# Kernel tuning notes

Hardware: AMD Instinct MI355X
Metric: run time of the kernel (lower is better)

The kernel has to match this reference:

```python
import jax, jax.numpy as jnp
import numpy as np

T, B, D = 2048, 2, 768
H = 8
HD = D // H
FFN = 3072
EPS = 1e-5


def layer_norm(x, g, b):
    mu = jnp.mean(x, axis=-1, keepdims=True)
    var = jnp.mean(jnp.square(x - mu), axis=-1, keepdims=True)
    return (x - mu) * jax.lax.rsqrt(var + EPS) * g + b


def setup_inputs() -> dict:
    key = jax.random.key(0)
    ks = jax.random.split(key, 12)
    s_d = 1.0 / np.sqrt(D)
    s_f = 1.0 / np.sqrt(FFN)
    return {
        "x": jax.random.normal(ks[0], (T, B, D), dtype=jnp.float32),
        "wq": jax.random.uniform(ks[1], (D, D), jnp.float32, -s_d, s_d),
        "bq": jnp.zeros((D,), jnp.float32),
        "wk": jax.random.uniform(ks[2], (D, D), jnp.float32, -s_d, s_d),
        "bk": jnp.zeros((D,), jnp.float32),
        "wv": jax.random.uniform(ks[3], (D, D), jnp.float32, -s_d, s_d),
        "bv": jnp.zeros((D,), jnp.float32),
        "wo": jax.random.uniform(ks[4], (D, D), jnp.float32, -s_d, s_d),
        "bo": jnp.zeros((D,), jnp.float32),
        "ln1_g": jnp.ones((D,), jnp.float32),
        "ln1_b": jnp.zeros((D,), jnp.float32),
        "w1": jax.random.uniform(ks[5], (FFN, D), jnp.float32, -s_d, s_d),
        "b1": jnp.zeros((FFN,), jnp.float32),
        "w2": jax.random.uniform(ks[6], (D, FFN), jnp.float32, -s_f, s_f),
        "b2": jnp.zeros((D,), jnp.float32),
        "ln2_g": jnp.ones((D,), jnp.float32),
        "ln2_b": jnp.zeros((D,), jnp.float32),
    }


def reference(x, wq, bq, wk, bk, wv, bv, wo, bo, ln1_g, ln1_b, w1, b1, w2, b2, ln2_g, ln2_b):
    # x: [T, B, D] (fairseq layout). Post-LN (layer_norm_first=False), relu, eval mode.
    residual = x
    q = (x @ wq.T + bq).reshape(T, B, H, HD)
    k = (x @ wk.T + bk).reshape(T, B, H, HD)
    v = (x @ wv.T + bv).reshape(T, B, H, HD)
    scale = 1.0 / np.sqrt(HD)
    scores = jnp.einsum('tbhd,sbhd->bhts', q, k) * scale  # [B,H,T,T]
    probs = jax.nn.softmax(scores, axis=-1)
    attn = jnp.einsum('bhts,sbhd->tbhd', probs, v).reshape(T, B, D)
    attn = attn @ wo.T + bo
    x = layer_norm(residual + attn, ln1_g, ln1_b)
    residual = x
    h = jax.nn.relu(x @ w1.T + b1)
    x = residual + (h @ w2.T + b2)
    x = layer_norm(x, ln2_g, ln2_b)
    return x
```

## Files before the change

### kernel.cpp

```cpp
#include <hip/hip_runtime.h>
#include <hip/hip_bf16.h>
#include <math.h>

constexpr int T_LEN = 2048;
constexpr int B_SZ  = 2;
constexpr int D_DIM = 768;
constexpr int H_NUM = 8;
constexpr int HD    = 96;
constexpr int FFN   = 3072;
constexpr float EPS = 1e-5f;
constexpr int TB    = T_LEN * B_SZ;
constexpr int QKV_LD = 3 * D_DIM;
constexpr int NSPLIT = 4;
constexpr int CHUNK  = T_LEN / NSPLIT;
constexpr float SC_LOG2E = 0.14724444458547f;

typedef __attribute__((ext_vector_type(8)))  short short8;
typedef __attribute__((ext_vector_type(4)))  short short4v;
typedef __attribute__((ext_vector_type(2)))  short short2v;
typedef __attribute__((ext_vector_type(4)))  float f32x4;
typedef __attribute__((ext_vector_type(16))) float f32x16;

__device__ __forceinline__ short f2bf(float f) {
    union { float f; unsigned u; } v; v.f = f;
    return (short)((v.u + 0x7FFFu + ((v.u >> 16) & 1u)) >> 16);
}
__device__ __forceinline__ float bf2f(short s) {
    union { unsigned u; float f; } v;
    v.u = ((unsigned)(unsigned short)s) << 16;
    return v.f;
}
__device__ __forceinline__ unsigned pkbf(float a, float b) {
    union { __hip_bfloat162 h; unsigned u; } v;
    v.h = __float22bfloat162_rn(make_float2(a, b));
    return v.u;
}

__device__ __forceinline__ void async_ld16(const short* g, short* l) {
    __builtin_amdgcn_global_load_lds(
        (const __attribute__((address_space(1))) unsigned int*)g,
        (__attribute__((address_space(3))) unsigned int*)l, 16, 0, 0);
}

struct CvtArgs {
    const float* src[7];
    short*       dst[7];
    float        scl[7];
    int          end4[7];
};

__global__ __launch_bounds__(256)
void cvt_all(CvtArgs a, int total4) {
    const int i = blockIdx.x * 256 + threadIdx.x;
    if (i >= total4) return;
    int s = 0;
    while (i >= a.end4[s]) ++s;
    const int base = s ? a.end4[s - 1] : 0;
    const int j = i - base;
    const float sc = a.scl[s];
    const float4 v = ((const float4*)a.src[s])[j];
    short4v o;
    o[0] = f2bf(v.x * sc); o[1] = f2bf(v.y * sc);
    o[2] = f2bf(v.z * sc); o[3] = f2bf(v.w * sc);
    *(short4v*)(a.dst[s] + (size_t)j * 4) = o;
}

__global__ __launch_bounds__(256)
void concat_bias(const float* __restrict__ bq, const float* __restrict__ bk,
                 const float* __restrict__ bv, float* __restrict__ dst) {
    const int i = blockIdx.x * 256 + threadIdx.x;
    if (i >= QKV_LD) return;
    dst[i] = (i < 768) ? bq[i] * SC_LOG2E : (i < 1536 ? bk[i - 768] : bv[i - 1536]);
}

template <int BM, int BN, typename OutT, bool RELU>
__global__ __launch_bounds__(256)
void gemm_mfma(const short* __restrict__ A, const short* __restrict__ W,
               const float* __restrict__ bias, OutT* __restrict__ C,
               int M, int N, int K) {
    constexpr int MI = BM / 32;
    constexpr int NI = BN / 32;
    __shared__ __align__(16) short As[BM * 32];
    __shared__ __align__(16) short Bs[BN * 32];

    const int tid  = threadIdx.x;
    const int w    = tid >> 6;
    const int lane = tid & 63;
    const int l16  = lane & 15;
    const int q4   = lane >> 4;
    const int row0 = blockIdx.y * BM;
    const int col0 = blockIdx.x * BN;
    const int wm   = (w >> 1) * (BM / 2);
    const int wn   = (w & 1) * (BN / 2);

    const short* gA0 = A + (size_t)(row0 + (tid >> 2)) * K + (tid & 3) * 8;
    const short* gA1 = gA0 + (size_t)64 * K;
    const short* gB0 = W + (size_t)(col0 + (tid >> 2)) * K + (tid & 3) * 8;
    const short* gB1 = gB0 + (size_t)64 * K;
    short* ldsA0 = As + w * 512;
    short* ldsA1 = As + 2048 + w * 512;
    short* ldsB0 = Bs + w * 512;
    short* ldsB1 = Bs + 2048 + w * 512;

    f32x4 acc[MI][NI];
#pragma unroll
    for (int mi = 0; mi < MI; ++mi)
#pragma unroll
        for (int ni = 0; ni < NI; ++ni)
#pragma unroll
            for (int r = 0; r < 4; ++r) acc[mi][ni][r] = 0.f;

    for (int k0 = 0; k0 < K; k0 += 32) {
        async_ld16(gA0, ldsA0);
        if constexpr (BM == 128) async_ld16(gA1, ldsA1);
        async_ld16(gB0, ldsB0);
        if constexpr (BN == 128) async_ld16(gB1, ldsB1);
        gA0 += 32; gB0 += 32;
        if constexpr (BM == 128) gA1 += 32;
        if constexpr (BN == 128) gB1 += 32;
        __syncthreads();

        short8 af[MI], bfr[NI];
#pragma unroll
        for (int mi = 0; mi < MI; ++mi)
            af[mi] = *(const short8*)&As[(wm + mi * 16 + l16) * 32 + q4 * 8];
#pragma unroll
        for (int ni = 0; ni < NI; ++ni)
            bfr[ni] = *(const short8*)&Bs[(wn + ni * 16 + l16) * 32 + q4 * 8];
#pragma unroll
        for (int mi = 0; mi < MI; ++mi)
#pragma unroll
            for (int ni = 0; ni < NI; ++ni)
                acc[mi][ni] = __builtin_amdgcn_mfma_f32_16x16x32_bf16(
                    af[mi], bfr[ni], acc[mi][ni], 0, 0, 0);
        __syncthreads();
    }

    float bcol[NI];
#pragma unroll
    for (int ni = 0; ni < NI; ++ni) bcol[ni] = bias[col0 + wn + ni * 16 + l16];
#pragma unroll
    for (int mi = 0; mi < MI; ++mi) {
#pragma unroll
        for (int r = 0; r < 4; ++r) {
            const int row = row0 + wm + mi * 16 + q4 * 4 + r;
#pragma unroll
            for (int ni = 0; ni < NI; ++ni) {
                float v = acc[mi][ni][r] + bcol[ni];
                if (RELU) v = fmaxf(v, 0.f);
                const int col = col0 + wn + ni * 16 + l16;
                if constexpr (sizeof(OutT) == 2)
                    C[(size_t)row * N + col] = (OutT)f2bf(v);
                else
                    C[(size_t)row * N + col] = v;
            }
        }
    }
}

__global__ __launch_bounds__(256)
void attn_mfma(const short* __restrict__ qkv, short* __restrict__ Opart,
               float* __restrict__ lpart) {
    __shared__ short Ks[2][32][56];
    __shared__ short Vt[128][44];
    __shared__ short Pw[4][32][36];

    const int tid  = threadIdx.x;
    const int w    = tid >> 6;
    const int lane = tid & 63;
    const int l31  = lane & 31;
    const int h5   = lane >> 5;
    const int t0   = blockIdx.x * 128;
    const int bh   = blockIdx.y;
    const int split = blockIdx.z;
    const int b    = bh >> 3;
    const int h    = bh & 7;

    for (int i = tid; i < 32 * 44; i += 256) {
        const int rr = i / 44, cc = i % 44;
        Vt[96 + rr][cc] = (rr == 0 && cc < 32) ? (short)0x3F80 : (short)0;
    }

    short8 qf[6];
    {
        const int qrow = t0 + w * 32 + l31;
        const short* qb = qkv + ((size_t)qrow * B_SZ + b) * QKV_LD + h * HD;
#pragma unroll
        for (int ks = 0; ks < 6; ++ks)
            qf[ks] = *(const short8*)&qb[ks * 16 + h5 * 8];
    }

    const int k_row = tid >> 2;
    const int k_q   = tid & 3;
    const short* gK = qkv + ((size_t)(split * CHUNK + k_row) * B_SZ + b) * QKV_LD
                      + D_DIM + h * HD + k_q * 24;
    const int ll = tid - 128;
    const int dg = (ll & 7) * 12;
    const int kg = (ll >> 3) * 2;
    const short* gV = qkv + ((size_t)(split * CHUNK + kg) * B_SZ + b) * QKV_LD
                      + 2 * D_DIM + h * HD + dg;
    const size_t step  = (size_t)32 * B_SZ * QKV_LD;
    const size_t vrow  = (size_t)B_SZ * QKV_LD;

    f32x16 oacc[4];
#pragma unroll
    for (int nt = 0; nt < 4; ++nt)
#pragma unroll
        for (int r = 0; r < 16; ++r) oacc[nt][r] = 0.f;

    short8  kpf[3];
    short4v vpf[2][3];
    if (w < 2) {
#pragma unroll
        for (int j = 0; j < 3; ++j) kpf[j] = *(const short8*)(gK + j * 8);
    } else {
#pragma unroll
        for (int r = 0; r < 2; ++r)
#pragma unroll
            for (int c = 0; c < 3; ++c)
                vpf[r][c] = *(const short4v*)(gV + r * vrow + c * 4);
    }

    for (int it = 0; it < CHUNK / 32; ++it) {
        __syncthreads();
        if (w < 2) {
#pragma unroll
            for (int j = 0; j < 3; ++j)
                *(short8*)&Ks[k_q >> 1][k_row][(k_q & 1) * 24 + j * 8] = kpf[j];
        } else {
#pragma unroll
            for (int d = 0; d < 12; ++d) {
                short2v t;
                t[0] = vpf[0][d >> 2][d & 3];
                t[1] = vpf[1][d >> 2][d & 3];
                *(short2v*)&Vt[dg + d][kg] = t;
            }
        }
        __syncthreads();

        if (it + 1 < CHUNK / 32) {
            const size_t off = (size_t)(it + 1) * step;
            if (w < 2) {
#pragma unroll
                for (int j = 0; j < 3; ++j)
                    kpf[j] = *(const short8*)(gK + off + j * 8);
            } else {
#pragma unroll
                for (int r = 0; r < 2; ++r)
#pragma unroll
                    for (int c = 0; c < 3; ++c)
                        vpf[r][c] = *(const short4v*)(gV + off + r * vrow + c * 4);
            }
        }

        f32x16 sa;
#pragma unroll
        for (int r = 0; r < 16; ++r) sa[r] = 0.f;
#pragma unroll
        for (int ks = 0; ks < 6; ++ks) {
            const int half = ks / 3;
            const int base = ks * 16 - half * 48;
            const short8 kf = *(const short8*)&Ks[half][l31][base + h5 * 8];
            sa = __builtin_amdgcn_mfma_f32_32x32x16_bf16(qf[ks], kf, sa, 0, 0, 0);
        }

        float pvx[16];
#pragma unroll
        for (int r = 0; r < 16; ++r) pvx[r] = __builtin_amdgcn_exp2f(sa[r]);
#pragma unroll
        for (int rp = 0; rp < 8; ++rp) {
            const unsigned u = pkbf(pvx[2 * rp], pvx[2 * rp + 1]);
            const int row = ((2 * rp) & 3) + 8 * ((2 * rp) >> 2) + 4 * h5;
            Pw[w][row][l31]     = (short)(u & 0xFFFFu);
            Pw[w][row + 1][l31] = (short)(u >> 16);
        }

#pragma unroll
        for (int ks2 = 0; ks2 < 2; ++ks2) {
            const short* pp = &Pw[w][l31][ks2 * 16 + h5 * 8];
            const short4v plo = *(const short4v*)pp;
            const short4v phi = *(const short4v*)(pp + 4);
            const short8 pfr = __builtin_shufflevector(plo, phi, 0, 1, 2, 3, 4, 5, 6, 7);
#pragma unroll
            for (int nt = 0; nt < 4; ++nt) {
                const short* vp = &Vt[nt * 32 + l31][ks2 * 16 + h5 * 8];
                const short4v vlo = *(const short4v*)vp;
                const short4v vhi = *(const short4v*)(vp + 4);
                const short8 vf = __builtin_shufflevector(vlo, vhi, 0, 1, 2, 3, 4, 5, 6, 7);
                oacc[nt] = __builtin_amdgcn_mfma_f32_32x32x16_bf16(pfr, vf, oacc[nt], 0, 0, 0);
            }
        }
    }

#pragma unroll
    for (int r = 0; r < 16; ++r) {
        const int row  = (r & 3) + 8 * (r >> 2) + 4 * h5;
        const int t    = t0 + w * 32 + row;
        const int grow = t * B_SZ + b;
        short* op = Opart + ((size_t)split * TB + grow) * D_DIM + h * HD;
#pragma unroll
        for (int nt = 0; nt < 3; ++nt)
            op[nt * 32 + l31] = f2bf(oacc[nt][r]);
        if (l31 == 0)
            lpart[((size_t)split * TB + grow) * H_NUM + h] = oacc[3][r];
    }
}

__global__ __launch_bounds__(256)
void attn_combine(const short* __restrict__ Opart, const float* __restrict__ lpart,
                  short* __restrict__ ctx) {
    const int row = blockIdx.x;
    const int tid = threadIdx.x;
    if (tid >= 192) return;
    const int d = tid * 4;
    const int h = d / 96;
    float o0 = 0.f, o1 = 0.f, o2 = 0.f, o3 = 0.f, l = 0.f;
#pragma unroll
    for (int c = 0; c < NSPLIT; ++c) {
        const short4v v = *(const short4v*)&Opart[((size_t)c * TB + row) * D_DIM + d];
        o0 += bf2f(v[0]); o1 += bf2f(v[1]); o2 += bf2f(v[2]); o3 += bf2f(v[3]);
        l += lpart[((size_t)c * TB + row) * H_NUM + h];
    }
    const float iv = 1.f / l;
    short4v r;
    r[0] = f2bf(o0 * iv); r[1] = f2bf(o1 * iv);
    r[2] = f2bf(o2 * iv); r[3] = f2bf(o3 * iv);
    *(short4v*)&ctx[(size_t)row * D_DIM + d] = r;
}

template <typename XT, typename OT>
__global__ __launch_bounds__(256)
void ln_residual(const XT* __restrict__ xres, const short* __restrict__ y,
                 const float* __restrict__ g, const float* __restrict__ bb,
                 OT* __restrict__ out) {
    const int row = blockIdx.x;
    const int tid = threadIdx.x;
    const XT*    xr = xres + (size_t)row * D_DIM;
    const short* yr = y + (size_t)row * D_DIM;

    float vals[3];
    float s = 0.f, s2 = 0.f;
#pragma unroll
    for (int i = 0; i < 3; ++i) {
        const int d = tid + i * 256;
        float xv;
        if constexpr (sizeof(XT) == 2) xv = bf2f((short)xr[d]);
        else                           xv = (float)xr[d];
        const float t = xv + bf2f(yr[d]);
        vals[i] = t;
        s += t;
        s2 = fmaf(t, t, s2);
    }
#pragma unroll
    for (int off = 32; off > 0; off >>= 1) {
        s  += __shfl_down(s, off);
        s2 += __shfl_down(s2, off);
    }
    __shared__ float red_s[4], red_s2[4];
    const int wid = tid >> 6, lane = tid & 63;
    if (lane == 0) { red_s[wid] = s; red_s2[wid] = s2; }
    __syncthreads();
    __shared__ float sh_mean, sh_rstd;
    if (tid == 0) {
        const float ts  = red_s[0] + red_s[1] + red_s[2] + red_s[3];
        const float ts2 = red_s2[0] + red_s2[1] + red_s2[2] + red_s2[3];
        const float mean = ts * (1.f / D_DIM);
        const float var  = ts2 * (1.f / D_DIM) - mean * mean;
        sh_mean = mean;
        sh_rstd = rsqrtf(var + EPS);
    }
    __syncthreads();
    const float mean = sh_mean, rstd = sh_rstd;
#pragma unroll
    for (int i = 0; i < 3; ++i) {
        const int d = tid + i * 256;
        const float o = (vals[i] - mean) * rstd * g[d] + bb[d];
        if constexpr (sizeof(OT) == 2)
            out[(size_t)row * D_DIM + d] = (OT)f2bf(o);
        else
            out[(size_t)row * D_DIM + d] = o;
    }
}

extern "C" void kernel_launch(void* const* d_in, const int* in_sizes, int n_in,
                              void* d_out, int out_size, void* d_ws, size_t ws_size,
                              hipStream_t stream) {
    const float* x     = (const float*)d_in[0];
    const float* wq    = (const float*)d_in[1];
    const float* bq    = (const float*)d_in[2];
    const float* wk    = (const float*)d_in[3];
    const float* bk    = (const float*)d_in[4];
    const float* wv    = (const float*)d_in[5];
    const float* bv    = (const float*)d_in[6];
    const float* wo    = (const float*)d_in[7];
    const float* bo    = (const float*)d_in[8];
    const float* ln1g  = (const float*)d_in[9];
    const float* ln1b  = (const float*)d_in[10];
    const float* w1    = (const float*)d_in[11];
    const float* b1    = (const float*)d_in[12];
    const float* w2    = (const float*)d_in[13];
    const float* b2    = (const float*)d_in[14];
    const float* ln2g  = (const float*)d_in[15];
    const float* ln2b  = (const float*)d_in[16];
    float* out = (float*)d_out;

    char* ws = (char*)d_ws;
    short* qkvb  = (short*)(ws + 0);
    short* ctxb  = (short*)(ws + 18874368);
    short* hb    = (short*)(ws + 0);
    short* xb    = (short*)(ws + 25165824);
    short* Opart = (short*)(ws + 25165824);
    float* lpart = (float*)(ws + 50331648);
    short* tmpb  = (short*)(ws + 25165824);
    short* x1b   = (short*)(ws + 31457280);
    short* wqkv  = (short*)(ws + 50855936);
    short* wob   = (short*)(ws + 54394880);
    short* w1b   = (short*)(ws + 55574528);
    short* w2b   = (short*)(ws + 60293120);
    float* bqkv  = (float*)(ws + 65011712);

    CvtArgs ca;
    ca.src[0] = x;  ca.dst[0] = xb;   ca.scl[0] = 1.f;
    ca.src[1] = wq; ca.dst[1] = wqkv; ca.scl[1] = SC_LOG2E;
    ca.src[2] = wk; ca.dst[2] = wqkv + 768 * 768;     ca.scl[2] = 1.f;
    ca.src[3] = wv; ca.dst[3] = wqkv + 2 * 768 * 768; ca.scl[3] = 1.f;
    ca.src[4] = wo; ca.dst[4] = wob;  ca.scl[4] = 1.f;
    ca.src[5] = w1; ca.dst[5] = w1b;  ca.scl[5] = 1.f;
    ca.src[6] = w2; ca.dst[6] = w2b;  ca.scl[6] = 1.f;
    const int n4[7] = {TB * D_DIM / 4, 768 * 768 / 4, 768 * 768 / 4, 768 * 768 / 4,
                       768 * 768 / 4, FFN * 768 / 4, 768 * FFN / 4};
    int acc4 = 0;
    for (int i = 0; i < 7; ++i) { acc4 += n4[i]; ca.end4[i] = acc4; }
    cvt_all<<<(acc4 + 255) / 256, 256, 0, stream>>>(ca, acc4);
    concat_bias<<<(QKV_LD + 255) / 256, 256, 0, stream>>>(bq, bk, bv, bqkv);

    gemm_mfma<128, 128, short, false><<<dim3(QKV_LD / 128, TB / 128), 256, 0, stream>>>(
        xb, wqkv, bqkv, qkvb, TB, QKV_LD, D_DIM);

    attn_mfma<<<dim3(T_LEN / 128, B_SZ * H_NUM, NSPLIT), dim3(256), 0, stream>>>(
        qkvb, Opart, lpart);
    attn_combine<<<dim3(TB), 256, 0, stream>>>(Opart, lpart, ctxb);

    gemm_mfma<64, 64, short, false><<<dim3(D_DIM / 64, TB / 64), 256, 0, stream>>>(
        ctxb, wob, bo, tmpb, TB, D_DIM, D_DIM);
    ln_residual<float, short><<<dim3(TB), 256, 0, stream>>>(x, tmpb, ln1g, ln1b, x1b);

    gemm_mfma<128, 128, short, true><<<dim3(FFN / 128, TB / 128), 256, 0, stream>>>(
        x1b, w1b, b1, hb, TB, FFN, D_DIM);
    gemm_mfma<64, 64, short, false><<<dim3(D_DIM / 64, TB / 64), 256, 0, stream>>>(
        hb, w2b, b2, tmpb, TB, D_DIM, FFN);
    ln_residual<short, float><<<dim3(TB), 256, 0, stream>>>(x1b, tmpb, ln2g, ln2b, out);
}
```

Before: 309.7 us.

## Double-buffer GEMM LDS tiles with async prefetch and deeper K for small tiles

Rewrites the GEMM main loop so LDS holds two buffers. The next K tile is issued asynchronously while the current one is computed, with a partial vmcnt wait and raw s_barrier instead of two __syncthreads per step. The 64x64 GEMMs now use BK=64, so every stage moves 4 async loads per thread and there are fewer loop iterations. This hides global load latency behind MFMA work, at the cost of twice the LDS footprint and possible LDS bank conflicts from the wider row stride.

```diff
diff --git a/kernel.cpp b/kernel.cpp
--- a/kernel.cpp
+++ b/kernel.cpp
@@ -73,15 +73,18 @@
     dst[i] = (i < 768) ? bq[i] * SC_LOG2E : (i < 1536 ? bk[i - 768] : bv[i - 1536]);
 }
 
-template <int BM, int BN, typename OutT, bool RELU>
+template <int BM, int BN, int BK, typename OutT, bool RELU>
 __global__ __launch_bounds__(256)
 void gemm_mfma(const short* __restrict__ A, const short* __restrict__ W,
                const float* __restrict__ bias, OutT* __restrict__ C,
                int M, int N, int K) {
     constexpr int MI = BM / 32;
     constexpr int NI = BN / 32;
-    __shared__ __align__(16) short As[BM * 32];
-    __shared__ __align__(16) short Bs[BN * 32];
+    constexpr int KI = BK / 32;
+    static_assert(BM * BK == 4096 && BN * BK == 4096, "4 glds/thread/stage");
+    constexpr int ROWSTEP = 2048 / BK;
+    __shared__ __align__(16) short As[2][4096];
+    __shared__ __align__(16) short Bs[2][4096];
 
     const int tid  = threadIdx.x;
     const int w    = tid >> 6;
@@ -93,14 +96,12 @@
     const int wm   = (w >> 1) * (BM / 2);
     const int wn   = (w & 1) * (BN / 2);
 
-    const short* gA0 = A + (size_t)(row0 + (tid >> 2)) * K + (tid & 3) * 8;
-    const short* gA1 = gA0 + (size_t)64 * K;
-    const short* gB0 = W + (size_t)(col0 + (tid >> 2)) * K + (tid & 3) * 8;
-    const short* gB1 = gB0 + (size_t)64 * K;
-    short* ldsA0 = As + w * 512;
-    short* ldsA1 = As + 2048 + w * 512;
-    short* ldsB0 = Bs + w * 512;
-    short* ldsB1 = Bs + 2048 + w * 512;
+    const int mA = tid / (BK / 8);
+    const int kA = (tid % (BK / 8)) * 8;
+    const short* gA0 = A + (size_t)(row0 + mA) * K + kA;
+    const short* gA1 = gA0 + (size_t)ROWSTEP * K;
+    const short* gB0 = W + (size_t)(col0 + mA) * K + kA;
+    const short* gB1 = gB0 + (size_t)ROWSTEP * K;
 
     f32x4 acc[MI][NI];
 #pragma unroll
@@ -110,30 +111,47 @@
 #pragma unroll
             for (int r = 0; r < 4; ++r) acc[mi][ni][r] = 0.f;
 
-    for (int k0 = 0; k0 < K; k0 += 32) {
-        async_ld16(gA0, ldsA0);
-        if constexpr (BM == 128) async_ld16(gA1, ldsA1);
-        async_ld16(gB0, ldsB0);
-        if constexpr (BN == 128) async_ld16(gB1, ldsB1);
-        gA0 += 32; gB0 += 32;
-        if constexpr (BM == 128) gA1 += 32;
-        if constexpr (BN == 128) gB1 += 32;
-        __syncthreads();
-
-        short8 af[MI], bfr[NI];
-#pragma unroll
-        for (int mi = 0; mi < MI; ++mi)
-            af[mi] = *(const short8*)&As[(wm + mi * 16 + l16) * 32 + q4 * 8];
-#pragma unroll
-        for (int ni = 0; ni < NI; ++ni)
-            bfr[ni] = *(const short8*)&Bs[(wn + ni * 16 + l16) * 32 + q4 * 8];
-#pragma unroll
-        for (int mi = 0; mi < MI; ++mi)
+    auto stage = [&](int buf) {
+        async_ld16(gA0, &As[buf][w * 512]);
+        async_ld16(gA1, &As[buf][2048 + w * 512]);
+        async_ld16(gB0, &Bs[buf][w * 512]);
+        async_ld16(gB1, &Bs[buf][2048 + w * 512]);
+        gA0 += BK; gA1 += BK; gB0 += BK; gB1 += BK;
+    };
+    auto compute = [&](int buf) {
+#pragma unroll
+        for (int ks = 0; ks < KI; ++ks) {
+            short8 af[MI], bfr[NI];
+#pragma unroll
+            for (int mi = 0; mi < MI; ++mi)
+                af[mi] = *(const short8*)&As[buf][(wm + mi * 16 + l16) * BK + ks * 32 + q4 * 8];
 #pragma unroll
             for (int ni = 0; ni < NI; ++ni)
-                acc[mi][ni] = __builtin_amdgcn_mfma_f32_16x16x32_bf16(
-                    af[mi], bfr[ni], acc[mi][ni], 0, 0, 0);
-        __syncthreads();
+                bfr[ni] = *(const short8*)&Bs[buf][(wn + ni * 16 + l16) * BK + ks * 32 + q4 * 8];
+#pragma unroll
+            for (int mi = 0; mi < MI; ++mi)
+#pragma unroll
+                for (int ni = 0; ni < NI; ++ni)
+                    acc[mi][ni] = __builtin_amdgcn_mfma_f32_16x16x32_bf16(
+                        af[mi], bfr[ni], acc[mi][ni], 0, 0, 0);
+        }
+    };
+
+    stage(0);
+    const int NT = K / BK;
+    for (int t = 0; t < NT; ++t) {
+        const int cur = t & 1;
+        if (t + 1 < NT) {
+            stage(cur ^ 1);
+            asm volatile("s_waitcnt vmcnt(4)" ::: "memory");
+        } else {
+            asm volatile("s_waitcnt vmcnt(0)" ::: "memory");
+        }
+        __builtin_amdgcn_s_barrier();
+        __builtin_amdgcn_sched_barrier(0);
+        compute(cur);
+        __builtin_amdgcn_s_barrier();
+        __builtin_amdgcn_sched_barrier(0);
     }
 
     float bcol[NI];
@@ -434,20 +452,20 @@
     cvt_all<<<(acc4 + 255) / 256, 256, 0, stream>>>(ca, acc4);
     concat_bias<<<(QKV_LD + 255) / 256, 256, 0, stream>>>(bq, bk, bv, bqkv);
 
-    gemm_mfma<128, 128, short, false><<<dim3(QKV_LD / 128, TB / 128), 256, 0, stream>>>(
+    gemm_mfma<128, 128, 32, short, false><<<dim3(QKV_LD / 128, TB / 128), 256, 0, stream>>>(
         xb, wqkv, bqkv, qkvb, TB, QKV_LD, D_DIM);
 
     attn_mfma<<<dim3(T_LEN / 128, B_SZ * H_NUM, NSPLIT), dim3(256), 0, stream>>>(
         qkvb, Opart, lpart);
     attn_combine<<<dim3(TB), 256, 0, stream>>>(Opart, lpart, ctxb);
 
-    gemm_mfma<64, 64, short, false><<<dim3(D_DIM / 64, TB / 64), 256, 0, stream>>>(
+    gemm_mfma<64, 64, 64, short, false><<<dim3(D_DIM / 64, TB / 64), 256, 0, stream>>>(
         ctxb, wob, bo, tmpb, TB, D_DIM, D_DIM);
     ln_residual<float, short><<<dim3(TB), 256, 0, stream>>>(x, tmpb, ln1g, ln1b, x1b);
 
-    gemm_mfma<128, 128, short, true><<<dim3(FFN / 128, TB / 128), 256, 0, stream>>>(
+    gemm_mfma<128, 128, 32, short, true><<<dim3(FFN / 128, TB / 128), 256, 0, stream>>>(
         x1b, w1b, b1, hb, TB, FFN, D_DIM);
-    gemm_mfma<64, 64, short, false><<<dim3(D_DIM / 64, TB / 64), 256, 0, stream>>>(
+    gemm_mfma<64, 64, 64, short, false><<<dim3(D_DIM / 64, TB / 64), 256, 0, stream>>>(
         hb, w2b, b2, tmpb, TB, D_DIM, FFN);
     ln_residual<short, float><<<dim3(TB), 256, 0, stream>>>(x1b, tmpb, ln2g, ln2b, out);
 }
```

New measurement: 300.0 us. -3.1%, faster.
